# Performance work log

Measured on AMD Instinct MI355X. Metric: run time of the kernel, lower is better.

## Reference

```python
import jax, jax.numpy as jnp
import numpy as np

TOPK = 8
EPS = 1e-12  # F.normalize eps


def setup_inputs() -> dict:
    key = jax.random.key(0)
    k1, k2 = jax.random.split(key)
    feats = jax.random.normal(k1, (4, 256, 64, 64), dtype=jnp.float32)
    logits = jax.random.normal(k2, (4, 1, 64, 64), dtype=jnp.float32)
    return {"feats": feats, "logits": logits}


def reference(feats, logits):
    b, c, h, w = feats.shape
    n = h * w
    feat_flat = feats.reshape(b, c, n)
    # F.normalize(dim=1): x / max(||x||_2, eps)
    norm = jnp.sqrt(jnp.sum(feat_flat * feat_flat, axis=1, keepdims=True))
    feat_norm = feat_flat / jnp.maximum(norm, EPS)
    # sim[b,i,j] = <f_i, f_j>  -> [B, N, N]
    sim = jnp.einsum('bci,bcj->bij', feat_norm, feat_norm)
    k = min(TOPK, n)
    _, idx = jax.lax.top_k(sim, k)  # [B, N, k] indices
    prob = jax.nn.sigmoid(logits).reshape(b, n)  # [B, N]
    # gathered[b,i,j] = prob[b, idx[b,i,j]]
    gathered = jax.vmap(lambda p, i: p[i])(prob, idx)  # [B, N, k]
    anchor = prob[:, :, None]  # [B, N, 1] broadcast over k
    loss = jnp.mean(jnp.abs(anchor - gathered))
    return loss
```

## Files before the change

### kernel.cpp

```cpp
#include <hip/hip_runtime.h>
#include <hip/hip_bf16.h>

typedef _Float16 half8 __attribute__((ext_vector_type(8)));
typedef unsigned short ushort8 __attribute__((ext_vector_type(8)));
typedef float floatx4 __attribute__((ext_vector_type(4)));

#define B_ 4
#define C_ 256
#define N_ 4096
#define NT 32
#define TRI 528

#define OFF_FN    ((size_t)0)
#define OFF_PROB  ((size_t)(8u << 20))
#define OFF_PART  (OFF_PROB + 65536)
#define OFF_TOP   ((size_t)(16u << 20))

__device__ __forceinline__ void gl_lds16(const void* g, void* l) {
    __builtin_amdgcn_global_load_lds(
        (const __attribute__((address_space(1))) void*)g,
        (__attribute__((address_space(3))) void*)l,
        16, 0, 0);
}

__device__ __forceinline__ void cas(uint32_t& a, uint32_t& b) {
    uint32_t hi = max(a, b); b = min(a, b); a = hi;
}

__device__ __forceinline__ void sort8(uint32_t v[8]) {
    cas(v[0],v[1]); cas(v[2],v[3]); cas(v[4],v[5]); cas(v[6],v[7]);
    cas(v[0],v[2]); cas(v[1],v[3]); cas(v[4],v[6]); cas(v[5],v[7]);
    cas(v[1],v[2]); cas(v[5],v[6]);
    cas(v[0],v[4]); cas(v[1],v[5]); cas(v[2],v[6]); cas(v[3],v[7]);
    cas(v[2],v[4]); cas(v[3],v[5]);
    cas(v[1],v[2]); cas(v[3],v[4]); cas(v[5],v[6]);
}

__device__ __forceinline__ void merge8(uint32_t r[8], const uint32_t n[8]) {
    uint32_t m[8];
#pragma unroll
    for (int i = 0; i < 8; ++i) m[i] = max(r[i], n[7 - i]);
    cas(m[0],m[4]); cas(m[1],m[5]); cas(m[2],m[6]); cas(m[3],m[7]);
    cas(m[0],m[2]); cas(m[1],m[3]); cas(m[4],m[6]); cas(m[5],m[7]);
    cas(m[0],m[1]); cas(m[2],m[3]); cas(m[4],m[5]); cas(m[6],m[7]);
#pragma unroll
    for (int i = 0; i < 8; ++i) r[i] = m[i];
}

#define TS 68
__global__ __launch_bounds__(256) void prep_kernel(const float* __restrict__ feats,
                                                   const float* __restrict__ logits,
                                                   _Float16* __restrict__ fn,
                                                   float* __restrict__ prob) {
    __shared__ __align__(16) float T[C_ * TS];
    __shared__ float S[256];
    __shared__ float I[64];

    const int t  = threadIdx.x;
    const int b  = blockIdx.x >> 6;
    const int i0 = (blockIdx.x & 63) * 64;
    const float* fb = feats + (size_t)b * C_ * N_;

#pragma unroll
    for (int k = 0; k < 16; ++k) {
        int ch = t + k * 256;
        int row = ch >> 4, col4 = ch & 15;
        float4 v = *(const float4*)(fb + (size_t)row * N_ + i0 + col4 * 4);
        *(float4*)&T[row * TS + col4 * 4] = v;
    }
    __syncthreads();
    {
        int i = t & 63, cq = t >> 6;
        float ss = 0.f;
#pragma unroll 8
        for (int j = 0; j < 64; ++j) { float v = T[(cq * 64 + j) * TS + i]; ss += v * v; }
        S[cq * 64 + i] = ss;
    }
    __syncthreads();
    if (t < 64) {
        float ss = S[t] + S[64 + t] + S[128 + t] + S[192 + t];
        I[t] = 1.f / fmaxf(sqrtf(ss), 1e-12f);
        float lg = logits[b * N_ + i0 + t];
        prob[b * N_ + i0 + t] = 1.f / (1.f + expf(-lg));
    }
    __syncthreads();
    {
        int i = t >> 2, chunk = t & 3;
        float s = I[i];
        _Float16* fr = fn + ((size_t)(b * N_ + i0 + i)) * C_ + chunk * 64;
#pragma unroll
        for (int v8 = 0; v8 < 8; ++v8) {
            half8 h;
#pragma unroll
            for (int e = 0; e < 8; ++e)
                h[e] = (_Float16)(T[(chunk * 64 + v8 * 8 + e) * TS + i] * s);
            *(half8*)(fr + v8 * 8) = h;
        }
    }
}

#define CSH 136
__global__ __launch_bounds__(256, 3) void gram_sel_kernel(const _Float16* __restrict__ fn,
                                                          uint32_t* __restrict__ top) {
    __shared__ __align__(16) char smem[128 * CSH * 2];
    _Float16* As = (_Float16*)smem;
    _Float16* Bs = (_Float16*)(smem + 16384);
    unsigned short* Ch = (unsigned short*)smem;
    uint32_t* Ms = (uint32_t*)smem;

    const int t    = threadIdx.x;
    const int lane = t & 63;
    const int w    = t >> 6;
    const int m16  = lane & 15;
    const int q    = lane >> 4;

    const int b = blockIdx.x / TRI;
    const int u = blockIdx.x - b * TRI;
    int it = (int)(32.5f - sqrtf(32.5f * 32.5f - 2.0f * (float)u));
    while (u >= (it + 1) * (65 - (it + 1)) / 2) ++it;
    while (u < it * (65 - it) / 2) --it;
    const int jt = it + (u - it * (65 - it) / 2);
    const bool diag = (it == jt);

    const int i0 = it * 128, j0 = jt * 128;
    const _Float16* fnb = fn + (size_t)b * N_ * C_;

    const int srowb = t >> 3;
    const int schunk = (t & 7) ^ (srowb & 7);
    const int sw = m16 & 7;

    floatx4 acc[2][8];
#pragma unroll
    for (int ri = 0; ri < 2; ++ri)
#pragma unroll
        for (int jj = 0; jj < 8; ++jj) acc[ri][jj] = floatx4{0.f, 0.f, 0.f, 0.f};

    for (int kc = 0; kc < 4; ++kc) {
#pragma unroll
        for (int r = 0; r < 4; ++r) {
            int row = r * 32 + srowb;
            const _Float16* gA = fnb + (size_t)(i0 + row) * C_ + kc * 64 + schunk * 8;
            const _Float16* gB = fnb + (size_t)(j0 + row) * C_ + kc * 64 + schunk * 8;
            gl_lds16(gA, (char*)As + r * 4096 + t * 16);
            gl_lds16(gB, (char*)Bs + r * 4096 + t * 16);
        }
        __syncthreads();
#pragma unroll
        for (int kk = 0; kk < 2; ++kk) {
            half8 a0 = *(const half8*)&As[(w * 32 + m16) * 64 + ((kk * 4 + q) ^ sw) * 8];
            half8 a1 = *(const half8*)&As[(w * 32 + 16 + m16) * 64 + ((kk * 4 + q) ^ sw) * 8];
#pragma unroll
            for (int jj = 0; jj < 8; ++jj) {
                half8 bf = *(const half8*)&Bs[(jj * 16 + m16) * 64 + ((kk * 4 + q) ^ sw) * 8];
                acc[0][jj] = __builtin_amdgcn_mfma_f32_16x16x32_f16(a0, bf, acc[0][jj], 0, 0, 0);
                acc[1][jj] = __builtin_amdgcn_mfma_f32_16x16x32_f16(a1, bf, acc[1][jj], 0, 0, 0);
            }
        }
        __syncthreads();
    }

#pragma unroll
    for (int jj = 0; jj < 8; ++jj)
#pragma unroll
        for (int ri = 0; ri < 2; ++ri) {
            const int col = jj * 16 + m16;
            const int row = w * 32 + ri * 16 + q * 4;
#pragma unroll
            for (int p = 0; p < 2; ++p) {
                auto pk2 = __builtin_amdgcn_cvt_pkrtz(acc[ri][jj][2 * p], acc[ri][jj][2 * p + 1]);
                uint32_t bits = __builtin_bit_cast(uint32_t, pk2);
                uint32_t s = (bits >> 15) & 0x00010001u;
                uint32_t fl = bits ^ (s * 0x7FFFu + 0x80008000u);
                *(uint32_t*)&Ch[col * CSH + row + 2 * p] = fl;
            }
        }
    __syncthreads();

    uint32_t cpk[8], rpk[8];
    {
        const int ccol = t >> 1, cr0 = (t & 1) * 64;
        const unsigned short* cc = &Ch[ccol * CSH + cr0];
        const int ibase = i0 + cr0;
#pragma unroll
        for (int g = 0; g < 8; ++g) {
            ushort8 v = *(const ushort8*)(cc + g * 8);
            uint32_t cand[8];
#pragma unroll
            for (int e = 0; e < 8; ++e)
                cand[e] = ((uint32_t)v[e] << 16) | (uint32_t)(ibase + g * 8 + e);
            sort8(cand);
            if (g == 0) {
#pragma unroll
                for (int s = 0; s < 8; ++s) cpk[s] = cand[s];
            } else merge8(cpk, cand);
        }
    }
    if (!diag) {
        const int rrow = t >> 1, ch0 = (t & 1) * 64;
        const unsigned short* cr = &Ch[ch0 * CSH + rrow];
        const int jbase = j0 + ch0;
#pragma unroll
        for (int g = 0; g < 8; ++g) {
            uint32_t cand[8];
#pragma unroll
            for (int e = 0; e < 8; ++e)
                cand[e] = ((uint32_t)cr[(g * 8 + e) * CSH] << 16) | (uint32_t)(jbase + g * 8 + e);
            sort8(cand);
            if (g == 0) {
#pragma unroll
                for (int s = 0; s < 8; ++s) rpk[s] = cand[s];
            } else merge8(rpk, cand);
        }
    }
    __syncthreads();

    if (t & 1) {
#pragma unroll
        for (int s = 0; s < 8; ++s) Ms[(t >> 1) * 8 + s] = cpk[s];
        if (!diag) {
#pragma unroll
            for (int s = 0; s < 8; ++s) Ms[1024 + (t >> 1) * 8 + s] = rpk[s];
        }
    }
    __syncthreads();
    if (!(t & 1)) {
        uint32_t o[8];
#pragma unroll
        for (int s = 0; s < 8; ++s) o[s] = Ms[(t >> 1) * 8 + s];
        merge8(cpk, o);
        uint32_t* dst = top + (((size_t)b * N_ + j0 + (t >> 1)) * 32 + it) * 8;
        *(uint4*)dst       = make_uint4(cpk[0], cpk[1], cpk[2], cpk[3]);
        *(uint4*)(dst + 4) = make_uint4(cpk[4], cpk[5], cpk[6], cpk[7]);
        if (!diag) {
#pragma unroll
            for (int s = 0; s < 8; ++s) o[s] = Ms[1024 + (t >> 1) * 8 + s];
            merge8(rpk, o);
            uint32_t* dst2 = top + (((size_t)b * N_ + i0 + (t >> 1)) * 32 + jt) * 8;
            *(uint4*)dst2       = make_uint4(rpk[0], rpk[1], rpk[2], rpk[3]);
            *(uint4*)(dst2 + 4) = make_uint4(rpk[4], rpk[5], rpk[6], rpk[7]);
        }
    }
}

__global__ __launch_bounds__(256) void merge_kernel(const uint32_t* __restrict__ top,
                                                    const float* __restrict__ prob,
                                                    float* __restrict__ partials) {
    __shared__ float red[4];
    const int t = threadIdx.x;
    const int lane = t & 63;
    const int w = t >> 6;
    const int rg = blockIdx.x * 4 + w;
    const int b = rg >> 12;

    uint4 v4 = ((const uint4*)(top + (size_t)rg * 256))[lane];
    uint32_t v[4] = {v4.x, v4.y, v4.z, v4.w};
    uint32_t m = max(max(v[0], v[1]), max(v[2], v[3]));

    const float* pb = prob + (b << 12);
    float p_r = prob[rg];
    float contrib = 0.f;
#pragma unroll
    for (int k = 0; k < 8; ++k) {
        uint32_t M = m;
#pragma unroll
        for (int off = 32; off; off >>= 1) M = max(M, (uint32_t)__shfl_xor((int)M, off));
        if (lane == k) contrib = fabsf(p_r - pb[M & 0xFFFu]);
#pragma unroll
        for (int s = 0; s < 4; ++s) v[s] = (v[s] == M) ? 0u : v[s];
        m = max(max(v[0], v[1]), max(v[2], v[3]));
    }
#pragma unroll
    for (int off = 32; off; off >>= 1) contrib += __shfl_xor(contrib, off);
    if (lane == 0) red[w] = contrib;
    __syncthreads();
    if (t == 0) partials[blockIdx.x] = red[0] + red[1] + red[2] + red[3];
}

__global__ __launch_bounds__(256) void final_kernel(const float* __restrict__ partials,
                                                    float* __restrict__ out) {
    __shared__ float red[256];
    int t = threadIdx.x;
    float s = 0.f;
#pragma unroll
    for (int k = 0; k < 16; ++k) s += partials[k * 256 + t];
    red[t] = s;
    __syncthreads();
    for (int off = 128; off > 0; off >>= 1) {
        if (t < off) red[t] += red[t + off];
        __syncthreads();
    }
    if (t == 0) out[0] = red[0] * (1.f / (B_ * N_ * 8.0f));
}

extern "C" void kernel_launch(void* const* d_in, const int* in_sizes, int n_in,
                              void* d_out, int out_size, void* d_ws, size_t ws_size,
                              hipStream_t stream) {
    const float* feats  = (const float*)d_in[0];
    const float* logits = (const float*)d_in[1];
    float* out = (float*)d_out;
    char* ws = (char*)d_ws;
    _Float16* fn   = (_Float16*)(ws + OFF_FN);
    float* prob    = (float*)(ws + OFF_PROB);
    float* parts   = (float*)(ws + OFF_PART);
    uint32_t* top  = (uint32_t*)(ws + OFF_TOP);

    prep_kernel<<<256, 256, 0, stream>>>(feats, logits, fn, prob);
    gram_sel_kernel<<<B_ * TRI, 256, 0, stream>>>(fn, top);
    merge_kernel<<<4096, 256, 0, stream>>>(top, prob, parts);
    final_kernel<<<1, 256, 0, stream>>>(parts, out);
}
```

Measured before the change: 122.7 us.

## Double-buffer gram K-loop, remap block order, widen prep kernel to 1024 threads

The gram kernel's K loop now runs as 8 steps of 32 channels with two LDS buffers, so the global-to-LDS loads for the next step are issued while MFMAs work on the current one. The XOR swizzle is rewritten to match the narrower rows. Block IDs are permuted (bid&7)*264 + bid>>3, which reorders how tiles are spread across the grid. The prep kernel is launched with 1024 threads per block instead of 256, giving each thread fewer loads and stores, though only a quarter of the threads take part in the norm reduction.

```diff
diff --git a/kernel.cpp b/kernel.cpp
--- a/kernel.cpp
+++ b/kernel.cpp
@@ -48,10 +48,10 @@
 }
 
 #define TS 68
-__global__ __launch_bounds__(256) void prep_kernel(const float* __restrict__ feats,
-                                                   const float* __restrict__ logits,
-                                                   _Float16* __restrict__ fn,
-                                                   float* __restrict__ prob) {
+__global__ __launch_bounds__(1024) void prep_kernel(const float* __restrict__ feats,
+                                                    const float* __restrict__ logits,
+                                                    _Float16* __restrict__ fn,
+                                                    float* __restrict__ prob) {
     __shared__ __align__(16) float T[C_ * TS];
     __shared__ float S[256];
     __shared__ float I[64];
@@ -62,14 +62,14 @@
     const float* fb = feats + (size_t)b * C_ * N_;
 
 #pragma unroll
-    for (int k = 0; k < 16; ++k) {
-        int ch = t + k * 256;
-        int row = ch >> 4, col4 = ch & 15;
+    for (int k = 0; k < 4; ++k) {
+        int idx = t + k * 1024;
+        int row = idx >> 4, col4 = idx & 15;
         float4 v = *(const float4*)(fb + (size_t)row * N_ + i0 + col4 * 4);
         *(float4*)&T[row * TS + col4 * 4] = v;
     }
     __syncthreads();
-    {
+    if (t < 256) {
         int i = t & 63, cq = t >> 6;
         float ss = 0.f;
 #pragma unroll 8
@@ -85,15 +85,15 @@
     }
     __syncthreads();
     {
-        int i = t >> 2, chunk = t & 3;
+        int i = t >> 4, sub = t & 15;
         float s = I[i];
-        _Float16* fr = fn + ((size_t)(b * N_ + i0 + i)) * C_ + chunk * 64;
-#pragma unroll
-        for (int v8 = 0; v8 < 8; ++v8) {
+        _Float16* fr = fn + ((size_t)(b * N_ + i0 + i)) * C_ + sub * 16;
+#pragma unroll
+        for (int v8 = 0; v8 < 2; ++v8) {
             half8 h;
 #pragma unroll
             for (int e = 0; e < 8; ++e)
-                h[e] = (_Float16)(T[(chunk * 64 + v8 * 8 + e) * TS + i] * s);
+                h[e] = (_Float16)(T[(sub * 16 + v8 * 8 + e) * TS + i] * s);
             *(half8*)(fr + v8 * 8) = h;
         }
     }
@@ -103,8 +103,6 @@
 __global__ __launch_bounds__(256, 3) void gram_sel_kernel(const _Float16* __restrict__ fn,
                                                           uint32_t* __restrict__ top) {
     __shared__ __align__(16) char smem[128 * CSH * 2];
-    _Float16* As = (_Float16*)smem;
-    _Float16* Bs = (_Float16*)(smem + 16384);
     unsigned short* Ch = (unsigned short*)smem;
     uint32_t* Ms = (uint32_t*)smem;
 
@@ -114,8 +112,11 @@
     const int m16  = lane & 15;
     const int q    = lane >> 4;
 
-    const int b = blockIdx.x / TRI;
-    const int u = blockIdx.x - b * TRI;
+    const int bid0 = blockIdx.x;
+    const int bid  = (bid0 & 7) * 264 + (bid0 >> 3);
+
+    const int b = bid / TRI;
+    const int u = bid - b * TRI;
     int it = (int)(32.5f - sqrtf(32.5f * 32.5f - 2.0f * (float)u));
     while (u >= (it + 1) * (65 - (it + 1)) / 2) ++it;
     while (u < it * (65 - it) / 2) --it;
@@ -125,9 +126,8 @@
     const int i0 = it * 128, j0 = jt * 128;
     const _Float16* fnb = fn + (size_t)b * N_ * C_;
 
-    const int srowb = t >> 3;
-    const int schunk = (t & 7) ^ (srowb & 7);
-    const int sw = m16 & 7;
+    const int rbase = t >> 2;
+    const int sch8  = ((t & 3) ^ (rbase & 3)) * 8;
 
     floatx4 acc[2][8];
 #pragma unroll
@@ -135,27 +135,37 @@
 #pragma unroll
         for (int jj = 0; jj < 8; ++jj) acc[ri][jj] = floatx4{0.f, 0.f, 0.f, 0.f};
 
-    for (int kc = 0; kc < 4; ++kc) {
-#pragma unroll
-        for (int r = 0; r < 4; ++r) {
-            int row = r * 32 + srowb;
-            const _Float16* gA = fnb + (size_t)(i0 + row) * C_ + kc * 64 + schunk * 8;
-            const _Float16* gB = fnb + (size_t)(j0 + row) * C_ + kc * 64 + schunk * 8;
-            gl_lds16(gA, (char*)As + r * 4096 + t * 16);
-            gl_lds16(gB, (char*)Bs + r * 4096 + t * 16);
-        }
-        __syncthreads();
-#pragma unroll
-        for (int kk = 0; kk < 2; ++kk) {
-            half8 a0 = *(const half8*)&As[(w * 32 + m16) * 64 + ((kk * 4 + q) ^ sw) * 8];
-            half8 a1 = *(const half8*)&As[(w * 32 + 16 + m16) * 64 + ((kk * 4 + q) ^ sw) * 8];
-#pragma unroll
-            for (int jj = 0; jj < 8; ++jj) {
-                half8 bf = *(const half8*)&Bs[(jj * 16 + m16) * 64 + ((kk * 4 + q) ^ sw) * 8];
-                acc[0][jj] = __builtin_amdgcn_mfma_f32_16x16x32_f16(a0, bf, acc[0][jj], 0, 0, 0);
-                acc[1][jj] = __builtin_amdgcn_mfma_f32_16x16x32_f16(a1, bf, acc[1][jj], 0, 0, 0);
-            }
-        }
+    auto stage = [&](int kc8, int bsel) {
+        char* base = smem + bsel * 16384;
+#pragma unroll
+        for (int rr = 0; rr < 2; ++rr) {
+            int row = rr * 64 + rbase;
+            const _Float16* gA = fnb + (size_t)(i0 + row) * C_ + kc8 * 32 + sch8;
+            const _Float16* gB = fnb + (size_t)(j0 + row) * C_ + kc8 * 32 + sch8;
+            gl_lds16(gA, base + rr * 4096 + t * 16);
+            gl_lds16(gB, base + 8192 + rr * 4096 + t * 16);
+        }
+    };
+    auto compute = [&](int bsel) {
+        const _Float16* Asb = (const _Float16*)(smem + bsel * 16384);
+        const _Float16* Bsb = Asb + 4096;
+        const int co = (q ^ (m16 & 3)) * 8;
+        half8 a0 = *(const half8*)&Asb[(w * 32 + m16) * 32 + co];
+        half8 a1 = *(const half8*)&Asb[(w * 32 + 16 + m16) * 32 + co];
+#pragma unroll
+        for (int jj = 0; jj < 8; ++jj) {
+            half8 bf = *(const half8*)&Bsb[(jj * 16 + m16) * 32 + co];
+            acc[0][jj] = __builtin_amdgcn_mfma_f32_16x16x32_f16(a0, bf, acc[0][jj], 0, 0, 0);
+            acc[1][jj] = __builtin_amdgcn_mfma_f32_16x16x32_f16(a1, bf, acc[1][jj], 0, 0, 0);
+        }
+    };
+
+    stage(0, 0);
+    __syncthreads();
+#pragma unroll
+    for (int s = 0; s < 8; ++s) {
+        if (s < 7) stage(s + 1, (s + 1) & 1);
+        compute(s & 1);
         __syncthreads();
     }
 
@@ -304,7 +314,7 @@
     float* parts   = (float*)(ws + OFF_PART);
     uint32_t* top  = (uint32_t*)(ws + OFF_TOP);
 
-    prep_kernel<<<256, 256, 0, stream>>>(feats, logits, fn, prob);
+    prep_kernel<<<256, 1024, 0, stream>>>(feats, logits, fn, prob);
     gram_sel_kernel<<<B_ * TRI, 256, 0, stream>>>(fn, top);
     merge_kernel<<<4096, 256, 0, stream>>>(top, prob, parts);
     final_kernel<<<1, 256, 0, stream>>>(parts, out);
```

Result: slower. 125.7 us (+2.4%).
